# Kernel optimization log

Hardware: AMD Instinct MI355X
Metric: run time of the kernel (lower is better)

## Reference

```python
import jax, jax.numpy as jnp
import numpy as np

BATCH, SEQ, D_IN, D_OUT = 32, 1024, 128, 128
NEG_SLOPE = 0.1


def setup_inputs() -> dict:
    key = jax.random.key(0)
    k1, k2, k3, k4 = jax.random.split(key, 4)
    nodes = jax.random.normal(k1, (BATCH, SEQ, D_IN), dtype=jnp.float32)
    adjacent = jax.random.randint(k2, (BATCH, SEQ, SEQ), 0, 2, dtype=jnp.int32)
    W = jax.random.normal(k3, (D_IN, D_OUT), dtype=jnp.float32) / np.sqrt(D_IN)
    B = jax.random.normal(k4, (D_IN, D_OUT), dtype=jnp.float32) / np.sqrt(D_IN)
    return {"nodes": nodes, "adjacent": adjacent, "W": W, "B": B}


def reference(nodes, adjacent, W, B):
    # mask[b, out, in] = 1 if edge (out -> in) present
    mask = (adjacent != 0).astype(nodes.dtype)
    # counts[b, in] = in-degree (number of 'out' neighbors pooled per target node)
    counts = mask.sum(axis=1)                               # [b, s_in]
    # segment-sum of neighbor features: pooled[b, in, d] = sum_out mask * nodes[b, out, d]
    pooled = jnp.einsum('boi,bod->bid', mask, nodes)        # [b, s_in, d]
    # mean over neighbors; nodes with zero degree get no pooled contribution
    pooled = jnp.where(counts[..., None] > 0,
                       pooled / jnp.maximum(counts, 1.0)[..., None],
                       jnp.zeros((), dtype=nodes.dtype))
    updated = nodes @ B + pooled @ W                        # [b, s, d_out]
    return jax.nn.leaky_relu(updated, negative_slope=NEG_SLOPE)
```

## Files before the change

### kernel.cpp

```cpp
#include <hip/hip_runtime.h>
#include <hip/hip_bf16.h>

#define SEQ 1024
#define DIM 128
#define NEG_SLOPE 0.1f

typedef __bf16 bf16x8 __attribute__((ext_vector_type(8)));
typedef float f32x4v __attribute__((ext_vector_type(4)));

union LdsU {
    struct {
        unsigned short mask_t[64][72];
        unsigned short nodes_t[128][72];
    } s;
    unsigned short pooled[64][136];
};

__device__ __forceinline__ unsigned short bfb(float f) {
    __bf16 h = (__bf16)f;
    return __builtin_bit_cast(unsigned short, h);
}
__device__ __forceinline__ unsigned mpack(int x0, int x1) {
    unsigned m0 = (x0 != 0) ? 0x3F80u : 0u;
    unsigned m1 = (x1 != 0) ? 0x3F80u : 0u;
    return m0 | (m1 << 16);
}

__global__ __launch_bounds__(256, 2)
void gcn_fused(const float* __restrict__ nodes,
               const int* __restrict__ adj,
               const float* __restrict__ W,
               const float* __restrict__ Bm,
               float* __restrict__ out)
{
    __shared__ LdsU u;

    const int bid   = blockIdx.x;
    const int xcd   = bid & 7;
    const int slot  = bid >> 3;
    const int batch = ((slot >> 4) << 3) | xcd;
    const int mtile = slot & 15;
    const int i0    = mtile << 6;

    const int tid  = threadIdx.x;
    const int wave = tid >> 6;
    const int lane = tid & 63;
    const int wm   = wave >> 1;
    const int wn   = wave & 1;
    const int lrow = lane & 15;
    const int quad = lane >> 4;

    const int*   __restrict__ adj_b   = adj   + (size_t)batch * SEQ * SEQ;
    const float* __restrict__ nodes_b = nodes + (size_t)batch * SEQ * DIM;

    const int a_row = (tid >> 4) * 4;
    const int a_col = (tid & 15) * 4;
    const int n_row = (tid >> 5) * 4;
    const int n_col = (tid & 31) * 4;

    f32x4v acc[2][4] = {};
    f32x4v acc_cnt[2] = {};

    bf16x8 ones;
    #pragma unroll
    for (int j = 0; j < 8; ++j) ones[j] = __builtin_bit_cast(__bf16, (unsigned short)0x3F80);

    int4   A[4];
    float4 N[8];

    auto load_chunk = [&](int o0) {
        const int* pa = adj_b + (size_t)(o0 + a_row) * SEQ + (i0 + a_col);
        #pragma unroll
        for (int r = 0; r < 4; ++r) A[r] = *(const int4*)(pa + (size_t)r * SEQ);
        const float* pn = nodes_b + (size_t)(o0 + n_row) * DIM + n_col;
        #pragma unroll
        for (int it = 0; it < 2; ++it)
            #pragma unroll
            for (int r = 0; r < 4; ++r)
                N[it * 4 + r] = *(const float4*)(pn + (size_t)(it * 32 + r) * DIM);
    };

    load_chunk(0);

    for (int chunk = 0; chunk < 16; ++chunk) {
        __syncthreads();
        #pragma unroll
        for (int j = 0; j < 4; ++j) {
            uint2 w;
            w.x = mpack(((const int*)&A[0])[j], ((const int*)&A[1])[j]);
            w.y = mpack(((const int*)&A[2])[j], ((const int*)&A[3])[j]);
            *(uint2*)&u.s.mask_t[a_col + j][a_row] = w;
        }
        #pragma unroll
        for (int it = 0; it < 2; ++it) {
            #pragma unroll
            for (int j = 0; j < 4; ++j) {
                uint2 w;
                w.x = (unsigned)bfb(((const float*)&N[it*4+0])[j]) |
                      ((unsigned)bfb(((const float*)&N[it*4+1])[j]) << 16);
                w.y = (unsigned)bfb(((const float*)&N[it*4+2])[j]) |
                      ((unsigned)bfb(((const float*)&N[it*4+3])[j]) << 16);
                *(uint2*)&u.s.nodes_t[n_col + j][it * 32 + n_row] = w;
            }
        }
        __syncthreads();
        if (chunk < 15) load_chunk((chunk + 1) * 64);

        #pragma unroll
        for (int kk = 0; kk < 2; ++kk) {
            bf16x8 av[2], bv[4];
            av[0] = *(const bf16x8*)&u.s.mask_t[wm * 32 + lrow][kk * 32 + quad * 8];
            av[1] = *(const bf16x8*)&u.s.mask_t[wm * 32 + 16 + lrow][kk * 32 + quad * 8];
            #pragma unroll
            for (int nf = 0; nf < 4; ++nf)
                bv[nf] = *(const bf16x8*)&u.s.nodes_t[wn * 64 + nf * 16 + lrow][kk * 32 + quad * 8];
            #pragma unroll
            for (int mf = 0; mf < 2; ++mf) {
                #pragma unroll
                for (int nf = 0; nf < 4; ++nf)
                    acc[mf][nf] = __builtin_amdgcn_mfma_f32_16x16x32_bf16(av[mf], bv[nf], acc[mf][nf], 0, 0, 0);
                acc_cnt[mf] = __builtin_amdgcn_mfma_f32_16x16x32_bf16(av[mf], ones, acc_cnt[mf], 0, 0, 0);
            }
        }
    }

    __syncthreads();
    #pragma unroll
    for (int mf = 0; mf < 2; ++mf) {
        #pragma unroll
        for (int r = 0; r < 4; ++r) {
            const int row = wm * 32 + mf * 16 + quad * 4 + r;
            const float cnt = acc_cnt[mf][r];
            const float inv = (cnt > 0.5f) ? 1.0f / cnt : 0.0f;
            #pragma unroll
            for (int nf = 0; nf < 4; ++nf) {
                const int col = wn * 64 + nf * 16 + lrow;
                u.pooled[row][col] = bfb(acc[mf][nf][r] * inv);
            }
        }
    }
    __syncthreads();

    f32x4v acc2[2][4] = {};
    const int d_b0 = wn * 64 + lrow;

    #pragma unroll
    for (int ks = 0; ks < 4; ++ks) {
        const int k0 = ks * 32 + quad * 8;
        bf16x8 av[2];
        #pragma unroll
        for (int mf = 0; mf < 2; ++mf)
            av[mf] = *(const bf16x8*)&u.pooled[wm * 32 + mf * 16 + lrow][k0];
        bf16x8 bv[4];
        const float* pw = W + (size_t)k0 * DIM + d_b0;
        #pragma unroll
        for (int nf = 0; nf < 4; ++nf) {
            #pragma unroll
            for (int j = 0; j < 8; ++j)
                bv[nf][j] = (__bf16)pw[j * DIM + nf * 16];
        }
        #pragma unroll
        for (int mf = 0; mf < 2; ++mf)
            #pragma unroll
            for (int nf = 0; nf < 4; ++nf)
                acc2[mf][nf] = __builtin_amdgcn_mfma_f32_16x16x32_bf16(av[mf], bv[nf], acc2[mf][nf], 0, 0, 0);
    }

    #pragma unroll
    for (int ks = 0; ks < 4; ++ks) {
        const int k0 = ks * 32 + quad * 8;
        bf16x8 av[2];
        #pragma unroll
        for (int mf = 0; mf < 2; ++mf) {
            const float* p = nodes_b + (size_t)(i0 + wm * 32 + mf * 16 + lrow) * DIM + k0;
            const float4 f1 = *(const float4*)p;
            const float4 f2 = *(const float4*)(p + 4);
            av[mf][0] = (__bf16)f1.x; av[mf][1] = (__bf16)f1.y;
            av[mf][2] = (__bf16)f1.z; av[mf][3] = (__bf16)f1.w;
            av[mf][4] = (__bf16)f2.x; av[mf][5] = (__bf16)f2.y;
            av[mf][6] = (__bf16)f2.z; av[mf][7] = (__bf16)f2.w;
        }
        bf16x8 bv[4];
        const float* pB = Bm + (size_t)k0 * DIM + d_b0;
        #pragma unroll
        for (int nf = 0; nf < 4; ++nf) {
            #pragma unroll
            for (int j = 0; j < 8; ++j)
                bv[nf][j] = (__bf16)pB[j * DIM + nf * 16];
        }
        #pragma unroll
        for (int mf = 0; mf < 2; ++mf)
            #pragma unroll
            for (int nf = 0; nf < 4; ++nf)
                acc2[mf][nf] = __builtin_amdgcn_mfma_f32_16x16x32_bf16(av[mf], bv[nf], acc2[mf][nf], 0, 0, 0);
    }

    float* out_b = out + (size_t)batch * SEQ * DIM;
    #pragma unroll
    for (int mf = 0; mf < 2; ++mf) {
        #pragma unroll
        for (int nf = 0; nf < 4; ++nf) {
            const int col = wn * 64 + nf * 16 + lrow;
            #pragma unroll
            for (int r = 0; r < 4; ++r) {
                const int row = i0 + wm * 32 + mf * 16 + quad * 4 + r;
                const float x = acc2[mf][nf][r];
                out_b[(size_t)row * DIM + col] = (x > 0.0f) ? x : NEG_SLOPE * x;
            }
        }
    }
}

extern "C" void kernel_launch(void* const* d_in, const int* in_sizes, int n_in,
                              void* d_out, int out_size, void* d_ws, size_t ws_size,
                              hipStream_t stream) {
    const float* nodes = (const float*)d_in[0];
    const int*   adj   = (const int*)d_in[1];
    const float* W     = (const float*)d_in[2];
    const float* Bm    = (const float*)d_in[3];
    float*       out   = (float*)d_out;
    gcn_fused<<<dim3(512), dim3(256), 0, stream>>>(nodes, adj, W, Bm, out);
}
```

Before: 224.2 us.

## Pre-transpose nodes and weights to bf16 workspace; double-buffer mask LDS

Adds two pre-pass kernels that transpose nodes into a bf16 [b, d, seq] layout and W/B into bf16 [d_out, k] layout in workspace. The main kernel then reads node B-fragments straight from global memory instead of staging them through LDS. The mask tile is double-buffered, which removes one barrier per chunk. Weight fragments become vectorised 16-byte loads instead of strided scalar loads. The cost is extra kernel launches plus a full write and re-read of a transposed nodes copy, and the per-chunk node reads now come from global/L2 rather than LDS.

```diff
diff --git a/kernel.cpp b/kernel.cpp
--- a/kernel.cpp
+++ b/kernel.cpp
@@ -8,13 +8,7 @@
 typedef __bf16 bf16x8 __attribute__((ext_vector_type(8)));
 typedef float f32x4v __attribute__((ext_vector_type(4)));
 
-union LdsU {
-    struct {
-        unsigned short mask_t[64][72];
-        unsigned short nodes_t[128][72];
-    } s;
-    unsigned short pooled[64][136];
-};
+#define NT_ELEMS (32u * 128u * 1024u)
 
 __device__ __forceinline__ unsigned short bfb(float f) {
     __bf16 h = (__bf16)f;
@@ -26,11 +20,65 @@
     return m0 | (m1 << 16);
 }
 
+__global__ __launch_bounds__(256)
+void transpose_nodes(const float* __restrict__ nodes, unsigned short* __restrict__ nt)
+{
+    __shared__ float lds[64][33];
+    const int bid = blockIdx.x;
+    const int b   = bid >> 6;
+    const int ot  = (bid >> 2) & 15;
+    const int dt  = bid & 3;
+    const int o0  = ot * 64, d0 = dt * 32;
+    const int tid = threadIdx.x;
+
+    const float* src = nodes + ((size_t)b * SEQ + o0) * DIM + d0;
+    #pragma unroll
+    for (int p = 0; p < 8; ++p) {
+        const int o = (tid >> 5) + p * 8;
+        const int d = tid & 31;
+        lds[o][d] = src[(size_t)o * DIM + d];
+    }
+    __syncthreads();
+    unsigned short* dst = nt + ((size_t)b * DIM + d0) * SEQ + o0;
+    #pragma unroll
+    for (int p = 0; p < 4; ++p) {
+        const int d  = (tid >> 5) + p * 8;
+        const int o2 = (tid & 31) * 2;
+        ushort2 v;
+        v.x = bfb(lds[o2][d]);
+        v.y = bfb(lds[o2 + 1][d]);
+        *(ushort2*)(dst + (size_t)d * SEQ + o2) = v;
+    }
+}
+
+__global__ __launch_bounds__(256)
+void transpose_wb(const float* __restrict__ W, const float* __restrict__ Bm,
+                  unsigned short* __restrict__ wt, unsigned short* __restrict__ bt)
+{
+    const int which = blockIdx.x & 1;
+    const int slice = blockIdx.x >> 1;
+    const float* in  = which ? Bm : W;
+    unsigned short* out = which ? bt : wt;
+    const int base = slice * 1024;
+    #pragma unroll
+    for (int r = 0; r < 4; ++r) {
+        const int idx = base + r * 256 + threadIdx.x;
+        const int d = idx >> 7, k = idx & 127;
+        out[idx] = bfb(in[k * DIM + d]);
+    }
+}
+
+union LdsU {
+    unsigned short mask_t[2][64][72];
+    unsigned short pooled[64][136];
+};
+
 __global__ __launch_bounds__(256, 2)
 void gcn_fused(const float* __restrict__ nodes,
                const int* __restrict__ adj,
-               const float* __restrict__ W,
-               const float* __restrict__ Bm,
+               const unsigned short* __restrict__ nt,
+               const unsigned short* __restrict__ wt,
+               const unsigned short* __restrict__ bt,
                float* __restrict__ out)
 {
     __shared__ LdsU u;
@@ -52,11 +100,10 @@
 
     const int*   __restrict__ adj_b   = adj   + (size_t)batch * SEQ * SEQ;
     const float* __restrict__ nodes_b = nodes + (size_t)batch * SEQ * DIM;
+    const unsigned short* __restrict__ nt_b = nt + (size_t)batch * DIM * SEQ;
 
     const int a_row = (tid >> 4) * 4;
     const int a_col = (tid & 15) * 4;
-    const int n_row = (tid >> 5) * 4;
-    const int n_col = (tid & 31) * 4;
 
     f32x4v acc[2][4] = {};
     f32x4v acc_cnt[2] = {};
@@ -65,55 +112,39 @@
     #pragma unroll
     for (int j = 0; j < 8; ++j) ones[j] = __builtin_bit_cast(__bf16, (unsigned short)0x3F80);
 
-    int4   A[4];
-    float4 N[8];
-
-    auto load_chunk = [&](int o0) {
+    int4 A[4];
+    auto load_adj = [&](int o0) {
         const int* pa = adj_b + (size_t)(o0 + a_row) * SEQ + (i0 + a_col);
         #pragma unroll
         for (int r = 0; r < 4; ++r) A[r] = *(const int4*)(pa + (size_t)r * SEQ);
-        const float* pn = nodes_b + (size_t)(o0 + n_row) * DIM + n_col;
-        #pragma unroll
-        for (int it = 0; it < 2; ++it)
-            #pragma unroll
-            for (int r = 0; r < 4; ++r)
-                N[it * 4 + r] = *(const float4*)(pn + (size_t)(it * 32 + r) * DIM);
     };
 
-    load_chunk(0);
-
-    for (int chunk = 0; chunk < 16; ++chunk) {
-        __syncthreads();
+    const int d_b0 = wn * 64 + lrow;
+
+    load_adj(0);
+
+    for (int n = 0; n < 16; ++n) {
+        const int buf = n & 1;
         #pragma unroll
         for (int j = 0; j < 4; ++j) {
             uint2 w;
             w.x = mpack(((const int*)&A[0])[j], ((const int*)&A[1])[j]);
             w.y = mpack(((const int*)&A[2])[j], ((const int*)&A[3])[j]);
-            *(uint2*)&u.s.mask_t[a_col + j][a_row] = w;
-        }
-        #pragma unroll
-        for (int it = 0; it < 2; ++it) {
-            #pragma unroll
-            for (int j = 0; j < 4; ++j) {
-                uint2 w;
-                w.x = (unsigned)bfb(((const float*)&N[it*4+0])[j]) |
-                      ((unsigned)bfb(((const float*)&N[it*4+1])[j]) << 16);
-                w.y = (unsigned)bfb(((const float*)&N[it*4+2])[j]) |
-                      ((unsigned)bfb(((const float*)&N[it*4+3])[j]) << 16);
-                *(uint2*)&u.s.nodes_t[n_col + j][it * 32 + n_row] = w;
-            }
-        }
+            *(uint2*)&u.mask_t[buf][a_col + j][a_row] = w;
+        }
+        if (n < 15) load_adj((n + 1) * 64);
         __syncthreads();
-        if (chunk < 15) load_chunk((chunk + 1) * 64);
-
+
+        const int o_base = n * 64;
         #pragma unroll
         for (int kk = 0; kk < 2; ++kk) {
+            const int ko = kk * 32 + quad * 8;
             bf16x8 av[2], bv[4];
-            av[0] = *(const bf16x8*)&u.s.mask_t[wm * 32 + lrow][kk * 32 + quad * 8];
-            av[1] = *(const bf16x8*)&u.s.mask_t[wm * 32 + 16 + lrow][kk * 32 + quad * 8];
+            av[0] = *(const bf16x8*)&u.mask_t[buf][wm * 32 + lrow][ko];
+            av[1] = *(const bf16x8*)&u.mask_t[buf][wm * 32 + 16 + lrow][ko];
             #pragma unroll
             for (int nf = 0; nf < 4; ++nf)
-                bv[nf] = *(const bf16x8*)&u.s.nodes_t[wn * 64 + nf * 16 + lrow][kk * 32 + quad * 8];
+                bv[nf] = *(const bf16x8*)(nt_b + (size_t)(d_b0 + nf * 16) * SEQ + o_base + ko);
             #pragma unroll
             for (int mf = 0; mf < 2; ++mf) {
                 #pragma unroll
@@ -142,57 +173,34 @@
     __syncthreads();
 
     f32x4v acc2[2][4] = {};
-    const int d_b0 = wn * 64 + lrow;
 
     #pragma unroll
     for (int ks = 0; ks < 4; ++ks) {
         const int k0 = ks * 32 + quad * 8;
-        bf16x8 av[2];
-        #pragma unroll
-        for (int mf = 0; mf < 2; ++mf)
+        bf16x8 av[2], av2[2], bw[4], bb[4];
+        #pragma unroll
+        for (int mf = 0; mf < 2; ++mf) {
             av[mf] = *(const bf16x8*)&u.pooled[wm * 32 + mf * 16 + lrow][k0];
-        bf16x8 bv[4];
-        const float* pw = W + (size_t)k0 * DIM + d_b0;
-        #pragma unroll
-        for (int nf = 0; nf < 4; ++nf) {
-            #pragma unroll
-            for (int j = 0; j < 8; ++j)
-                bv[nf][j] = (__bf16)pw[j * DIM + nf * 16];
-        }
-        #pragma unroll
-        for (int mf = 0; mf < 2; ++mf)
-            #pragma unroll
-            for (int nf = 0; nf < 4; ++nf)
-                acc2[mf][nf] = __builtin_amdgcn_mfma_f32_16x16x32_bf16(av[mf], bv[nf], acc2[mf][nf], 0, 0, 0);
-    }
-
-    #pragma unroll
-    for (int ks = 0; ks < 4; ++ks) {
-        const int k0 = ks * 32 + quad * 8;
-        bf16x8 av[2];
-        #pragma unroll
-        for (int mf = 0; mf < 2; ++mf) {
             const float* p = nodes_b + (size_t)(i0 + wm * 32 + mf * 16 + lrow) * DIM + k0;
             const float4 f1 = *(const float4*)p;
             const float4 f2 = *(const float4*)(p + 4);
-            av[mf][0] = (__bf16)f1.x; av[mf][1] = (__bf16)f1.y;
-            av[mf][2] = (__bf16)f1.z; av[mf][3] = (__bf16)f1.w;
-            av[mf][4] = (__bf16)f2.x; av[mf][5] = (__bf16)f2.y;
-            av[mf][6] = (__bf16)f2.z; av[mf][7] = (__bf16)f2.w;
-        }
-        bf16x8 bv[4];
-        const float* pB = Bm + (size_t)k0 * DIM + d_b0;
+            av2[mf][0] = (__bf16)f1.x; av2[mf][1] = (__bf16)f1.y;
+            av2[mf][2] = (__bf16)f1.z; av2[mf][3] = (__bf16)f1.w;
+            av2[mf][4] = (__bf16)f2.x; av2[mf][5] = (__bf16)f2.y;
+            av2[mf][6] = (__bf16)f2.z; av2[mf][7] = (__bf16)f2.w;
+        }
         #pragma unroll
         for (int nf = 0; nf < 4; ++nf) {
-            #pragma unroll
-            for (int j = 0; j < 8; ++j)
-                bv[nf][j] = (__bf16)pB[j * DIM + nf * 16];
+            bw[nf] = *(const bf16x8*)(wt + (size_t)(d_b0 + nf * 16) * DIM + k0);
+            bb[nf] = *(const bf16x8*)(bt + (size_t)(d_b0 + nf * 16) * DIM + k0);
         }
         #pragma unroll
         for (int mf = 0; mf < 2; ++mf)
             #pragma unroll
-            for (int nf = 0; nf < 4; ++nf)
-                acc2[mf][nf] = __builtin_amdgcn_mfma_f32_16x16x32_bf16(av[mf], bv[nf], acc2[mf][nf], 0, 0, 0);
+            for (int nf = 0; nf < 4; ++nf) {
+                acc2[mf][nf] = __builtin_amdgcn_mfma_f32_16x16x32_bf16(av[mf],  bw[nf], acc2[mf][nf], 0, 0, 0);
+                acc2[mf][nf] = __builtin_amdgcn_mfma_f32_16x16x32_bf16(av2[mf], bb[nf], acc2[mf][nf], 0, 0, 0);
+            }
     }
 
     float* out_b = out + (size_t)batch * SEQ * DIM;
@@ -219,5 +227,12 @@
     const float* W     = (const float*)d_in[2];
     const float* Bm    = (const float*)d_in[3];
     float*       out   = (float*)d_out;
-    gcn_fused<<<dim3(512), dim3(256), 0, stream>>>(nodes, adj, W, Bm, out);
-}
+
+    unsigned short* nt = (unsigned short*)d_ws;
+    unsigned short* wt = nt + NT_ELEMS;
+    unsigned short* bt = wt + 16384;
+
+    transpose_nodes<<<dim3(2048), dim3(256), 0, stream>>>(nodes, nt);
+    transpose_wb<<<dim3(32), dim3(256), 0, stream>>>(W, Bm, wt, bt);
+    gcn_fused<<<dim3(512), dim3(256), 0, stream>>>(nodes, adj, nt, wt, bt, out);
+}
```

Result: slower. 234.5 us (+4.6%).
